# Optimization experiments

Measured on AMD Instinct MI355X. Metric: run time of the kernel, lower is better.

## Reference

```python
import jax, jax.numpy as jnp
import numpy as np
import math

B, C, D, H, W = 1, 64, 16, 16, 16
HEADS = 4
HD = C // HEADS  # head_dim = 16


def conv3d(x, w, b, pad):
    # x: [B,C,D,H,W], w: [O,I,kd,kh,kw], pad: (pd,ph,pw)
    y = jax.lax.conv_general_dilated(
        x, w, window_strides=(1, 1, 1),
        padding=[(p, p) for p in pad],
        dimension_numbers=('NCDHW', 'OIDHW', 'NCDHW'))
    return y + b[None, :, None, None, None]


def setup_inputs() -> dict:
    key = jax.random.key(0)
    ks = jax.random.split(key, 10)
    s = 0.02
    return {
        'x': jax.random.normal(ks[0], (B, C, D, H, W), jnp.float32),
        'gamma': jax.random.normal(ks[1], (1,), jnp.float32),
        'w_sp': jax.random.normal(ks[2], (C, C, 1, 3, 3), jnp.float32) * s,
        'b_sp': jax.random.normal(ks[3], (C,), jnp.float32) * s,
        'w_spec': jax.random.normal(ks[4], (C, C, 3, 1, 1), jnp.float32) * s,
        'b_spec': jax.random.normal(ks[5], (C,), jnp.float32) * s,
        'w_qkv': jax.random.normal(ks[6], (3 * C, C, 1, 1, 1), jnp.float32) * s,
        'b_qkv': jax.random.normal(ks[7], (3 * C,), jnp.float32) * s,
        'w_proj': jax.random.normal(ks[8], (C, C, 1, 1, 1), jnp.float32) * s,
        'b_proj': jax.random.normal(ks[9], (C,), jnp.float32) * s,
    }


def _decay_exponent(dtype):
    # Faithful to the torch permute quirk (requires H == W):
    # exponent[i,j,k,m,n,o] = |i-m| + |j-k| + |n-o|
    dd = jnp.abs(jnp.arange(D)[:, None] - jnp.arange(D)[None, :]).astype(dtype)  # [D,D]
    hh = jnp.abs(jnp.arange(H)[:, None] - jnp.arange(H)[None, :]).astype(dtype)  # [H,H]
    ww = jnp.abs(jnp.arange(W)[:, None] - jnp.arange(W)[None, :]).astype(dtype)  # [W,W]
    return (dd[:, None, None, :, None, None]      # i (axis0), m (axis3)
            + hh[None, :, :, None, None, None]    # j (axis1), k (axis2)
            + ww[None, None, None, None, :, :])   # n (axis4), o (axis5)


def _forward(x, gamma, w_sp, b_sp, w_spec, b_spec, w_qkv, b_qkv, w_proj, b_proj):
    x = conv3d(x, w_sp, b_sp, (0, 1, 1))
    x = conv3d(x, w_spec, b_spec, (1, 0, 0))
    qkv = conv3d(x, w_qkv, b_qkv, (0, 0, 0))
    q, k, v = jnp.split(qkv, 3, axis=1)
    rs = lambda t: t.reshape(B, HEADS, HD, D, H, W)
    q, k, v = rs(q), rs(k), rs(v)

    g = jax.nn.sigmoid(gamma[0])
    decay = g ** _decay_exponent(x.dtype)  # [D,H,W,D,W,W] (H==W)

    # attn[b,h,i,j,k,m,n,o]: (i,j,k)=query D,H,W ; (m,n,o)=key D,H,W
    attn = jnp.einsum('bhdijk,bhdmno->bhijkmno', q, k) / math.sqrt(HD)
    attn = jax.nn.softmax(attn * decay, axis=-1)  # softmax over key-W axis o only
    out = jnp.einsum('bhijkmno,bhdmno->bhdijk', attn, v)
    out = out.reshape(B, C, D, H, W)
    return conv3d(out, w_proj, b_proj, (0, 0, 0))


def reference(x, gamma, w_sp, b_sp, w_spec, b_spec, w_qkv, b_qkv, w_proj, b_proj):
    return _forward(x, gamma, w_sp, b_sp, w_spec, b_spec, w_qkv, b_qkv, w_proj, b_proj)
```

## Files before the change

kernel.cpp:

```cpp
#include <hip/hip_runtime.h>
#include <math.h>

#define CN   262144
#define BTP 196
#define PTP 68

typedef __attribute__((ext_vector_type(8))) short short8;
typedef __attribute__((ext_vector_type(4))) short short4v;
typedef __attribute__((ext_vector_type(4))) float float4v;

static __device__ __forceinline__ unsigned short f2bf(float f) {
    union { float f; unsigned u; } v; v.f = f;
    unsigned r = (v.u + 0x7FFFu + ((v.u >> 16) & 1u)) >> 16;
    return (unsigned short)r;
}

static __device__ __forceinline__ unsigned ld_u32g(const void* p) {
    return __hip_atomic_load((const unsigned*)p, __ATOMIC_RELAXED,
                             __HIP_MEMORY_SCOPE_AGENT);
}
static __device__ __forceinline__ void st_u32g(void* p, unsigned v) {
    __hip_atomic_store((unsigned*)p, v, __ATOMIC_RELAXED,
                       __HIP_MEMORY_SCOPE_AGENT);
}
static __device__ __forceinline__ float ld_f32g(const void* p) {
    return __hip_atomic_load((const float*)p, __ATOMIC_RELAXED,
                             __HIP_MEMORY_SCOPE_AGENT);
}
static __device__ __forceinline__ void st_f32g(void* p, float v) {
    __hip_atomic_store((float*)p, v, __ATOMIC_RELAXED,
                       __HIP_MEMORY_SCOPE_AGENT);
}

#define BAR_LIMIT (1 << 20)

static __device__ __forceinline__ void grid_bar(int* arrive, int* release, int phase) {
    __syncthreads();
    if (blockIdx.x == 0) {
        if (threadIdx.x < 64) {
            if (threadIdx.x == 0)
                __hip_atomic_store(&arrive[0], phase,
                                   __ATOMIC_RELAXED, __HIP_MEMORY_SCOPE_AGENT);
            int base = (int)threadIdx.x * 8 * 32;
            int z = 0; bool done = false;
            while (!done && z < BAR_LIMIT) {
                int mn = phase;
                #pragma unroll
                for (int q = 0; q < 8; ++q) {
                    int a = __hip_atomic_load(&arrive[base + q * 32],
                                              __ATOMIC_RELAXED, __HIP_MEMORY_SCOPE_AGENT);
                    mn = (a < mn) ? a : mn;
                }
                done = (mn >= phase);
                if (!done) __builtin_amdgcn_s_sleep(1);
                ++z;
            }
            __hip_atomic_store(&release[(int)threadIdx.x * 32], phase,
                               __ATOMIC_RELAXED, __HIP_MEMORY_SCOPE_AGENT);
        }
        __syncthreads();
    } else {
        if (threadIdx.x == 0) {
            __hip_atomic_store(&arrive[(int)blockIdx.x * 32], phase,
                               __ATOMIC_RELAXED, __HIP_MEMORY_SCOPE_AGENT);
            int* rel = &release[(blockIdx.x & 63) * 32];
            int z = 0;
            while (__hip_atomic_load(rel, __ATOMIC_RELAXED,
                                     __HIP_MEMORY_SCOPE_AGENT) < phase
                   && z < BAR_LIMIT) {
                __builtin_amdgcn_s_sleep(8);
                ++z;
            }
        }
        __syncthreads();
    }
}

__global__ __launch_bounds__(512, 4) void mega_kernel(
        const float* __restrict__ x, const float* __restrict__ gamma,
        const float* __restrict__ w_sp, const float* __restrict__ b_sp,
        const float* __restrict__ w_spec, const float* __restrict__ b_spec,
        const float* __restrict__ w_qkv, const float* __restrict__ b_qkv,
        const float* __restrict__ w_proj, const float* __restrict__ b_proj,
        float* __restrict__ out, float* ws, int* arrive, int* release) {
    __shared__ __align__(16) unsigned char lds_raw[32896];

    float* y1  = ws;
    unsigned short* wfb = (unsigned short*)(ws + CN);
    float* bfv = ws + CN + 20480;
    unsigned short* qb  = (unsigned short*)(ws + 2 * CN);
    unsigned short* kb  = (unsigned short*)(ws + 2 * CN + CN / 2);
    unsigned short* vtb = (unsigned short*)(ws + 3 * CN);
    float* aoall = ws + 3 * CN + CN / 2;

    if (blockIdx.x < 256) {
        unsigned short* Bt = (unsigned short*)lds_raw;
        int d = blockIdx.x >> 4;
        int h = blockIdx.x & 15;
        int tid = threadIdx.x;
        bool act = tid < 256;
        int px = tid & 15, cig = (tid >> 4) & 15;

        float rcur[12], rnxt[12];
        #define LOAD_CHUNK(dh_, rr)                                            \
            {                                                                  \
                int hh = h + (dh_) - 1;                                        \
                _Pragma("unroll")                                              \
                for (int cc = 0; cc < 4; ++cc) {                               \
                    int ci = cig * 4 + cc;                                     \
                    const float* xr = x + ci * 4096 + d * 256 + hh * 16;       \
                    _Pragma("unroll")                                          \
                    for (int dw = 0; dw < 3; ++dw) {                           \
                        int ww = px + dw - 1;                                  \
                        float v = 0.f;                                         \
                        if (hh >= 0 && hh <= 15 && ww >= 0 && ww <= 15)        \
                            v = xr[ww];                                        \
                        (rr)[cc * 3 + dw] = v;                                 \
                    }                                                          \
                }                                                              \
            }

        if (act) LOAD_CHUNK(0, rcur);

        int wv = (tid >> 6) & 3, lane = tid & 63;
        int quad = lane >> 4, l15 = lane & 15;
        float4v acc = {0.f, 0.f, 0.f, 0.f};
        const float* wrow = w_sp + (wv * 16 + l15) * 576;

        #pragma unroll
        for (int c = 0; c < 3; ++c) {
            __syncthreads();
            if (act) {
                #pragma unroll
                for (int cc = 0; cc < 4; ++cc) {
                    int ci = cig * 4 + cc;
                    Bt[px * BTP + ci * 3 + 0] = f2bf(rcur[cc * 3 + 0]);
                    Bt[px * BTP + ci * 3 + 1] = f2bf(rcur[cc * 3 + 1]);
                    Bt[px * BTP + ci * 3 + 2] = f2bf(rcur[cc * 3 + 2]);
                }
            }
            __syncthreads();
            if (act) {
                if (c < 2) LOAD_CHUNK(c + 1, rnxt);

                const unsigned short* brow = Bt + l15 * BTP + quad * 8;
                #pragma unroll
                for (int ks = 0; ks < 6; ++ks) {
                    short8 af;
                    #pragma unroll
                    for (int j = 0; j < 8; ++j) {
                        int kp = quad * 8 + ks * 32 + j;
                        af[j] = (short)f2bf(wrow[c * 3 + (kp / 3) * 9 + (kp % 3)]);
                    }
                    short4v lo = *(const short4v*)(brow + ks * 32);
                    short4v hi = *(const short4v*)(brow + ks * 32 + 4);
                    short8 bf8 = {lo[0], lo[1], lo[2], lo[3], hi[0], hi[1], hi[2], hi[3]};
                    acc = __builtin_amdgcn_mfma_f32_16x16x32_bf16(af, bf8, acc, 0, 0, 0);
                }
                #pragma unroll
                for (int q2 = 0; q2 < 12; ++q2) rcur[q2] = rnxt[q2];
            }
        }

        if (act) {
            int p = d * 256 + h * 16 + l15;
            #pragma unroll
            for (int r = 0; r < 4; ++r) {
                int co = wv * 16 + quad * 4 + r;
                st_f32g(y1 + co * 4096 + p, acc[r] + b_sp[co]);
            }
        }
        #undef LOAD_CHUNK
    } else {
        int idx = (blockIdx.x - 256) * 512 + threadIdx.x;
        if (idx < 18432) {
            int oc = idx / 96;
            int rp = idx % 96;
            int r0 = rp * 2;
            float s0 = 0.f, s1 = 0.f;
            #pragma unroll 8
            for (int ci = 0; ci < 64; ++ci) {
                float wq = w_qkv[oc * 64 + ci];
                s0 += wq * w_spec[ci * 192 + r0];
                s1 += wq * w_spec[ci * 192 + r0 + 1];
            }
            if (oc < 64) { s0 *= 0.25f; s1 *= 0.25f; }
            st_u32g(wfb + oc * 192 + r0,
                    (unsigned)f2bf(s0) | ((unsigned)f2bf(s1) << 16));
        } else if (idx < 18432 + 192) {
            int j = idx - 18432;
            float t = b_qkv[j];
            for (int ci = 0; ci < 64; ++ci) t += w_qkv[j * 64 + ci] * b_spec[ci];
            if (j < 64) t *= 0.25f;
            st_f32g(bfv + j, t);
        }
    }
    grid_bar(arrive, release, 1);

    if (blockIdx.x < 384) {
        unsigned short* Bt = (unsigned short*)lds_raw;
        int bI  = blockIdx.x;
        int ocg = bI % 3;
        int pq  = (bI / 3) & 7;
        int d   = bI / 24;
        int tid = threadIdx.x;

        {
            int px  = tid & 31;
            int cig = tid >> 5;
            const float* yb = y1 + d * 256 + pq * 32 + px;
            #pragma unroll
            for (int cc = 0; cc < 4; ++cc) {
                int ci = cig * 4 + cc;
                const float* yc = yb + ci * 4096;
                #pragma unroll
                for (int t = 0; t < 3; ++t) {
                    float v = 0.f;
                    if (!((d == 0 && t == 0) || (d == 15 && t == 2)))
                        v = ld_f32g(yc + (t - 1) * 256);
                    Bt[px * BTP + ci * 3 + t] = f2bf(v);
                }
            }
        }

        int wv = tid >> 6, lane = tid & 63;
        int quad = lane >> 4, l15 = lane & 15;
        int Mt = wv >> 1;
        int nt = wv & 1;

        short8 af[6];
        {
            const unsigned* ab = (const unsigned*)(wfb + (ocg * 64 + Mt * 16 + l15) * 192)
                                 + quad * 4;
            #pragma unroll
            for (int ks = 0; ks < 6; ++ks) {
                union { unsigned u[4]; short8 s8; } t;
                #pragma unroll
                for (int q = 0; q < 4; ++q) t.u[q] = ld_u32g(ab + ks * 16 + q);
                af[ks] = t.s8;
            }
        }
        float bias[4];
        #pragma unroll
        for (int r = 0; r < 4; ++r)
            bias[r] = ld_f32g(bfv + ocg * 64 + Mt * 16 + quad * 4 + r);

        __syncthreads();

        float4v czero = {0.f, 0.f, 0.f, 0.f};
        float4v acc = czero;
        {
            const unsigned short* brow = Bt + (nt * 16 + l15) * BTP + quad * 8;
            #pragma unroll
            for (int ks = 0; ks < 6; ++ks) {
                short4v lo = *(const short4v*)(brow + ks * 32);
                short4v hi = *(const short4v*)(brow + ks * 32 + 4);
                short8 bf8 = {lo[0], lo[1], lo[2], lo[3], hi[0], hi[1], hi[2], hi[3]};
                acc = __builtin_amdgcn_mfma_f32_16x16x32_bf16(af[ks], bf8, acc, 0, 0, 0);
            }
        }

        {
            int p = d * 256 + pq * 32 + nt * 16 + l15;
            if (ocg == 2) {
                int h = (p >> 4) & 15, w0 = p & 15;
                int kap = 8 * (w0 >> 2) + 4 * (h & 1) + (w0 & 3);
                unsigned short* dstb = vtb + ((Mt * 16 + d) * 8 + (h >> 1)) * 512
                                           + (quad * 4) * 32;
                int odd = l15 & 1;
                int kap_e = kap - odd;
                #pragma unroll
                for (int r = 0; r < 4; ++r) {
                    unsigned self = f2bf(acc[r] + bias[r]);
                    unsigned other = (unsigned)__shfl_xor((int)self, 1) & 0xFFFFu;
                    unsigned pk = odd ? (other | (self << 16)) : (self | (other << 16));
                    if ((r < 2) == (odd != 0)) continue;
                    st_u32g(dstb + r * 32 + kap_e, pk);
                }
            } else {
                unsigned short* dst = (ocg == 0 ? qb : kb) + Mt * 65536 + p * 16 + quad * 4;
                unsigned t0 = (unsigned)f2bf(acc[0] + bias[0])
                            | ((unsigned)f2bf(acc[1] + bias[1]) << 16);
                unsigned t1 = (unsigned)f2bf(acc[2] + bias[2])
                            | ((unsigned)f2bf(acc[3] + bias[3]) << 16);
                st_u32g(dst, t0);
                st_u32g(dst + 2, t1);
            }
        }
    }
    grid_bar(arrive, release, 2);

    {
        unsigned short* KSH = (unsigned short*)lds_raw;
        unsigned short* VSH = (unsigned short*)lds_raw + 8192;
        float* gp = (float*)(lds_raw + 32768);
        int tid = threadIdx.x;
        if (tid < 32) {
            float g = 1.f / (1.f + __expf(-gamma[0]));
            gp[tid] = __powf(g, (float)tid);
        }
        int wv = tid >> 6, lane = tid & 63;
        int quad = lane >> 4, l15 = lane & 15;
        short8 zero8 = {0, 0, 0, 0, 0, 0, 0, 0};
        float4v czero = {0.f, 0.f, 0.f, 0.f};

        #pragma unroll 1
        for (int it = 0; it < 2; ++it) {
            int bI = blockIdx.x + it * 512;
            int head = bI >> 8;
            int mg   = (bI >> 5) & 7;
            int oct  = bI & 31;
            int t = oct * 8 + wv;
            int i = t >> 4, j = t & 15;

            short8 qf = zero8;
            if (quad < 2) {
                const unsigned* qrow = (const unsigned*)(qb + head * 65536
                                        + (t * 16 + l15) * 16) + quad * 4;
                union { unsigned u[4]; short8 s8; } qt;
                #pragma unroll
                for (int q = 0; q < 4; ++q) qt.u[q] = ld_u32g(qrow + q);
                qf = qt.s8;
            }

            const unsigned* kbu = (const unsigned*)(kb  + head * 65536 + mg * 2 * 4096);
            const unsigned* vbu = (const unsigned*)(vtb + head * 65536 + mg * 2 * 4096);
            unsigned kv[16];
            #pragma unroll
            for (int q = 0; q < 4; ++q) kv[q]      = ld_u32g(kbu + tid * 4 + q);
            #pragma unroll
            for (int q = 0; q < 4; ++q) kv[4 + q]  = ld_u32g(vbu + tid * 4 + q);
            #pragma unroll
            for (int q = 0; q < 4; ++q) kv[8 + q]  = ld_u32g(kbu + 2048 + tid * 4 + q);
            #pragma unroll
            for (int q = 0; q < 4; ++q) kv[12 + q] = ld_u32g(vbu + 2048 + tid * 4 + q);
            __syncthreads();
            #pragma unroll
            for (int q = 0; q < 4; ++q) {
                ((unsigned*)KSH)[tid * 4 + q]        = kv[q];
                ((unsigned*)VSH)[tid * 4 + q]        = kv[4 + q];
                ((unsigned*)(KSH + 4096))[tid * 4 + q] = kv[8 + q];
                ((unsigned*)(VSH + 4096))[tid * 4 + q] = kv[12 + q];
            }
            __syncthreads();

            float wd[4];
            #pragma unroll
            for (int r = 0; r < 4; ++r)
                wd[r] = gp[abs(l15 - (quad * 4 + r))] * 1.4426950408889634f;

            float4v O = czero;
            #pragma unroll
            for (int mm = 0; mm < 2; ++mm) {
                int m = mg * 2 + mm;
                const unsigned short* kk = KSH + mm * 4096;
                const unsigned short* vv = VSH + mm * 4096;
                int eim = abs(i - m);
                #pragma unroll
                for (int np = 0; np < 8; ++np) {
                    union { unsigned u[4]; short8 s8; } a2u;
                    #pragma unroll
                    for (int s = 0; s < 2; ++s) {
                        int n = np * 2 + s;
                        short8 a1 = zero8;
                        if (quad < 2)
                            a1 = *(const short8*)(kk + n * 256 + l15 * 16 + quad * 8);
                        float4v d1 = __builtin_amdgcn_mfma_f32_16x16x32_bf16(a1, qf, czero, 0, 0, 0);
                        float smn = gp[eim + abs(j - n)];
                        float e0 = __builtin_amdgcn_exp2f(d1[0] * smn * wd[0]);
                        float e1 = __builtin_amdgcn_exp2f(d1[1] * smn * wd[1]);
                        float e2 = __builtin_amdgcn_exp2f(d1[2] * smn * wd[2]);
                        float e3 = __builtin_amdgcn_exp2f(d1[3] * smn * wd[3]);
                        float sm = e0 + e1 + e2 + e3;
                        sm += __shfl_xor(sm, 16);
                        sm += __shfl_xor(sm, 32);
                        float inv = __builtin_amdgcn_rcpf(sm);
                        union { float f; unsigned u; } p0, p1, p2, p3;
                        p0.f = e0 * inv; p1.f = e1 * inv;
                        p2.f = e2 * inv; p3.f = e3 * inv;
                        a2u.u[s * 2]     = ((p0.u + 0x8000u) >> 16) | ((p1.u + 0x8000u) & 0xFFFF0000u);
                        a2u.u[s * 2 + 1] = ((p2.u + 0x8000u) >> 16) | ((p3.u + 0x8000u) & 0xFFFF0000u);
                    }
                    short8 b2 = *(const short8*)(vv + np * 512 + l15 * 32 + quad * 8);
                    O = __builtin_amdgcn_mfma_f32_16x16x32_bf16(a2u.s8, b2, O, 0, 0, 0);
                }
            }

            float* aop = aoall + mg * CN + (head * 16 + l15) * 4096 + t * 16 + quad * 4;
            #pragma unroll
            for (int r = 0; r < 4; ++r) st_f32g(aop + r, O[r]);
        }
    }
    grid_bar(arrive, release, 3);

    if (blockIdx.x < 256) {
        unsigned short* Bt = (unsigned short*)lds_raw;
        int d   = blockIdx.x >> 4;
        int p16 = blockIdx.x & 15;
        int tid = threadIdx.x;
        bool act = tid < 256;

        if (act) {
            int px = tid & 15, cig = (tid >> 4) & 15;
            int gbase = d * 256 + p16 * 16 + px;
            #pragma unroll
            for (int cc = 0; cc < 4; ++cc) {
                int ci = cig * 4 + cc;
                int ga = ci * 4096 + gbase;
                float v = 0.f;
                #pragma unroll
                for (int k = 0; k < 8; ++k) v += ld_f32g(aoall + k * CN + ga);
                Bt[px * PTP + ci] = f2bf(v);
            }
        }
        __syncthreads();

        if (act) {
            int wv = (tid >> 6) & 3, lane = tid & 63;
            int quad = lane >> 4, l15 = lane & 15;
            float4v czero = {0.f, 0.f, 0.f, 0.f};
            float4v acc = czero;

            short8 af[2];
            const float* wsrc = w_proj + (wv * 16 + l15) * 64 + quad * 8;
            #pragma unroll
            for (int ks = 0; ks < 2; ++ks) {
                float4 wa = *(const float4*)(wsrc + ks * 32);
                float4 wb = *(const float4*)(wsrc + ks * 32 + 4);
                short8 a8 = {(short)f2bf(wa.x), (short)f2bf(wa.y), (short)f2bf(wa.z),
                             (short)f2bf(wa.w), (short)f2bf(wb.x), (short)f2bf(wb.y),
                             (short)f2bf(wb.z), (short)f2bf(wb.w)};
                af[ks] = a8;
            }
            const unsigned short* brow = Bt + l15 * PTP + quad * 8;
            #pragma unroll
            for (int ks = 0; ks < 2; ++ks) {
                short4v lo = *(const short4v*)(brow + ks * 32);
                short4v hi = *(const short4v*)(brow + ks * 32 + 4);
                short8 bf8 = {lo[0], lo[1], lo[2], lo[3], hi[0], hi[1], hi[2], hi[3]};
                acc = __builtin_amdgcn_mfma_f32_16x16x32_bf16(af[ks], bf8, acc, 0, 0, 0);
            }

            int p = d * 256 + p16 * 16 + l15;
            #pragma unroll
            for (int r = 0; r < 4; ++r) {
                int oc = wv * 16 + quad * 4 + r;
                out[oc * 4096 + p] = acc[r] + b_proj[oc];
            }
        }
    }
}

extern "C" void kernel_launch(void* const* d_in, const int* in_sizes, int n_in,
                              void* d_out, int out_size, void* d_ws, size_t ws_size,
                              hipStream_t stream) {
    const float* x      = (const float*)d_in[0];
    const float* gamma  = (const float*)d_in[1];
    const float* w_sp   = (const float*)d_in[2];
    const float* b_sp   = (const float*)d_in[3];
    const float* w_spec = (const float*)d_in[4];
    const float* b_spec = (const float*)d_in[5];
    const float* w_qkv  = (const float*)d_in[6];
    const float* b_qkv  = (const float*)d_in[7];
    const float* w_proj = (const float*)d_in[8];
    const float* b_proj = (const float*)d_in[9];
    float* out = (float*)d_out;
    float* ws = (float*)d_ws;

    int* arrive  = (int*)(ws + 12 * CN);
    int* release = arrive + 512 * 32;
    hipMemsetAsync(arrive, 0, (512 + 64) * 128, stream);

    mega_kernel<<<dim3(512), dim3(512), 0, stream>>>(
        x, gamma, w_sp, b_sp, w_spec, b_spec, w_qkv, b_qkv, w_proj, b_proj,
        out, ws, arrive, release);
}
```

Measured before the change: 146.1 us.

## Restructure attention stage to one pass per block with four key slices and plain loads

```diff
diff --git a/kernel.cpp b/kernel.cpp
--- a/kernel.cpp
+++ b/kernel.cpp
@@ -15,17 +15,13 @@
     return (unsigned short)r;
 }
 
-static __device__ __forceinline__ unsigned ld_u32g(const void* p) {
-    return __hip_atomic_load((const unsigned*)p, __ATOMIC_RELAXED,
-                             __HIP_MEMORY_SCOPE_AGENT);
-}
 static __device__ __forceinline__ void st_u32g(void* p, unsigned v) {
     __hip_atomic_store((unsigned*)p, v, __ATOMIC_RELAXED,
                        __HIP_MEMORY_SCOPE_AGENT);
 }
-static __device__ __forceinline__ float ld_f32g(const void* p) {
-    return __hip_atomic_load((const float*)p, __ATOMIC_RELAXED,
-                             __HIP_MEMORY_SCOPE_AGENT);
+static __device__ __forceinline__ void st_u64g(void* p, unsigned long long v) {
+    __hip_atomic_store((unsigned long long*)p, v, __ATOMIC_RELAXED,
+                       __HIP_MEMORY_SCOPE_AGENT);
 }
 static __device__ __forceinline__ void st_f32g(void* p, float v) {
     __hip_atomic_store((float*)p, v, __ATOMIC_RELAXED,
@@ -68,7 +64,7 @@
             while (__hip_atomic_load(rel, __ATOMIC_RELAXED,
                                      __HIP_MEMORY_SCOPE_AGENT) < phase
                    && z < BAR_LIMIT) {
-                __builtin_amdgcn_s_sleep(8);
+                __builtin_amdgcn_s_sleep(2);
                 ++z;
             }
         }
@@ -217,7 +213,7 @@
                 for (int t = 0; t < 3; ++t) {
                     float v = 0.f;
                     if (!((d == 0 && t == 0) || (d == 15 && t == 2)))
-                        v = ld_f32g(yc + (t - 1) * 256);
+                        v = yc[(t - 1) * 256];
                     Bt[px * BTP + ci * 3 + t] = f2bf(v);
                 }
             }
@@ -230,20 +226,13 @@
 
         short8 af[6];
         {
-            const unsigned* ab = (const unsigned*)(wfb + (ocg * 64 + Mt * 16 + l15) * 192)
-                                 + quad * 4;
-            #pragma unroll
-            for (int ks = 0; ks < 6; ++ks) {
-                union { unsigned u[4]; short8 s8; } t;
-                #pragma unroll
-                for (int q = 0; q < 4; ++q) t.u[q] = ld_u32g(ab + ks * 16 + q);
-                af[ks] = t.s8;
-            }
+            const unsigned short* ab = wfb + (ocg * 64 + Mt * 16 + l15) * 192 + quad * 8;
+            #pragma unroll
+            for (int ks = 0; ks < 6; ++ks) af[ks] = *(const short8*)(ab + ks * 32);
         }
         float bias[4];
         #pragma unroll
-        for (int r = 0; r < 4; ++r)
-            bias[r] = ld_f32g(bfv + ocg * 64 + Mt * 16 + quad * 4 + r);
+        for (int r = 0; r < 4; ++r) bias[r] = bfv[ocg * 64 + Mt * 16 + quad * 4 + r];
 
         __syncthreads();
 
@@ -283,8 +272,7 @@
                             | ((unsigned)f2bf(acc[1] + bias[1]) << 16);
                 unsigned t1 = (unsigned)f2bf(acc[2] + bias[2])
                             | ((unsigned)f2bf(acc[3] + bias[3]) << 16);
-                st_u32g(dst, t0);
-                st_u32g(dst + 2, t1);
+                st_u64g(dst, (unsigned long long)t0 | ((unsigned long long)t1 << 32));
             }
         }
     }
@@ -292,104 +280,85 @@
 
     {
         unsigned short* KSH = (unsigned short*)lds_raw;
-        unsigned short* VSH = (unsigned short*)lds_raw + 8192;
         float* gp = (float*)(lds_raw + 32768);
         int tid = threadIdx.x;
+        int bI = blockIdx.x;
+        int head = bI >> 7;
+        int mg   = (bI >> 5) & 3;
+        int oct  = bI & 31;
+
         if (tid < 32) {
             float g = 1.f / (1.f + __expf(-gamma[0]));
             gp[tid] = __powf(g, (float)tid);
         }
+
         int wv = tid >> 6, lane = tid & 63;
         int quad = lane >> 4, l15 = lane & 15;
+        int t = oct * 8 + wv;
+        int i = t >> 4, j = t & 15;
+
         short8 zero8 = {0, 0, 0, 0, 0, 0, 0, 0};
         float4v czero = {0.f, 0.f, 0.f, 0.f};
-
+        short8 qf = zero8;
+        if (quad < 2)
+            qf = *(const short8*)(qb + head * 65536 + (t * 16 + l15) * 16 + quad * 8);
+
+        {
+            const float4* kbh = (const float4*)(kb + head * 65536 + mg * 4 * 4096);
+            #pragma unroll
+            for (int q = 0; q < 4; ++q)
+                ((float4*)KSH)[q * 512 + tid] = kbh[q * 512 + tid];
+        }
+        __syncthreads();
+
+        float wd[4];
+        #pragma unroll
+        for (int r = 0; r < 4; ++r)
+            wd[r] = gp[abs(l15 - (quad * 4 + r))] * 1.4426950408889634f;
+
+        float4v O = czero;
         #pragma unroll 1
-        for (int it = 0; it < 2; ++it) {
-            int bI = blockIdx.x + it * 512;
-            int head = bI >> 8;
-            int mg   = (bI >> 5) & 7;
-            int oct  = bI & 31;
-            int t = oct * 8 + wv;
-            int i = t >> 4, j = t & 15;
-
-            short8 qf = zero8;
-            if (quad < 2) {
-                const unsigned* qrow = (const unsigned*)(qb + head * 65536
-                                        + (t * 16 + l15) * 16) + quad * 4;
-                union { unsigned u[4]; short8 s8; } qt;
-                #pragma unroll
-                for (int q = 0; q < 4; ++q) qt.u[q] = ld_u32g(qrow + q);
-                qf = qt.s8;
-            }
-
-            const unsigned* kbu = (const unsigned*)(kb  + head * 65536 + mg * 2 * 4096);
-            const unsigned* vbu = (const unsigned*)(vtb + head * 65536 + mg * 2 * 4096);
-            unsigned kv[16];
-            #pragma unroll
-            for (int q = 0; q < 4; ++q) kv[q]      = ld_u32g(kbu + tid * 4 + q);
-            #pragma unroll
-            for (int q = 0; q < 4; ++q) kv[4 + q]  = ld_u32g(vbu + tid * 4 + q);
-            #pragma unroll
-            for (int q = 0; q < 4; ++q) kv[8 + q]  = ld_u32g(kbu + 2048 + tid * 4 + q);
-            #pragma unroll
-            for (int q = 0; q < 4; ++q) kv[12 + q] = ld_u32g(vbu + 2048 + tid * 4 + q);
-            __syncthreads();
-            #pragma unroll
-            for (int q = 0; q < 4; ++q) {
-                ((unsigned*)KSH)[tid * 4 + q]        = kv[q];
-                ((unsigned*)VSH)[tid * 4 + q]        = kv[4 + q];
-                ((unsigned*)(KSH + 4096))[tid * 4 + q] = kv[8 + q];
-                ((unsigned*)(VSH + 4096))[tid * 4 + q] = kv[12 + q];
-            }
-            __syncthreads();
-
-            float wd[4];
-            #pragma unroll
-            for (int r = 0; r < 4; ++r)
-                wd[r] = gp[abs(l15 - (quad * 4 + r))] * 1.4426950408889634f;
-
-            float4v O = czero;
-            #pragma unroll
-            for (int mm = 0; mm < 2; ++mm) {
-                int m = mg * 2 + mm;
-                const unsigned short* kk = KSH + mm * 4096;
-                const unsigned short* vv = VSH + mm * 4096;
-                int eim = abs(i - m);
-                #pragma unroll
-                for (int np = 0; np < 8; ++np) {
-                    union { unsigned u[4]; short8 s8; } a2u;
-                    #pragma unroll
-                    for (int s = 0; s < 2; ++s) {
-                        int n = np * 2 + s;
-                        short8 a1 = zero8;
-                        if (quad < 2)
-                            a1 = *(const short8*)(kk + n * 256 + l15 * 16 + quad * 8);
-                        float4v d1 = __builtin_amdgcn_mfma_f32_16x16x32_bf16(a1, qf, czero, 0, 0, 0);
-                        float smn = gp[eim + abs(j - n)];
-                        float e0 = __builtin_amdgcn_exp2f(d1[0] * smn * wd[0]);
-                        float e1 = __builtin_amdgcn_exp2f(d1[1] * smn * wd[1]);
-                        float e2 = __builtin_amdgcn_exp2f(d1[2] * smn * wd[2]);
-                        float e3 = __builtin_amdgcn_exp2f(d1[3] * smn * wd[3]);
-                        float sm = e0 + e1 + e2 + e3;
-                        sm += __shfl_xor(sm, 16);
-                        sm += __shfl_xor(sm, 32);
-                        float inv = __builtin_amdgcn_rcpf(sm);
-                        union { float f; unsigned u; } p0, p1, p2, p3;
-                        p0.f = e0 * inv; p1.f = e1 * inv;
-                        p2.f = e2 * inv; p3.f = e3 * inv;
-                        a2u.u[s * 2]     = ((p0.u + 0x8000u) >> 16) | ((p1.u + 0x8000u) & 0xFFFF0000u);
-                        a2u.u[s * 2 + 1] = ((p2.u + 0x8000u) >> 16) | ((p3.u + 0x8000u) & 0xFFFF0000u);
-                    }
-                    short8 b2 = *(const short8*)(vv + np * 512 + l15 * 32 + quad * 8);
-                    O = __builtin_amdgcn_mfma_f32_16x16x32_bf16(a2u.s8, b2, O, 0, 0, 0);
-                }
-            }
-
-            float* aop = aoall + mg * CN + (head * 16 + l15) * 4096 + t * 16 + quad * 4;
-            #pragma unroll
-            for (int r = 0; r < 4; ++r) st_f32g(aop + r, O[r]);
-        }
+        for (int mm = 0; mm < 4; ++mm) {
+            int m = mg * 4 + mm;
+            const unsigned short* kk = KSH + mm * 4096;
+            const unsigned short* vvg = vtb + head * 65536 + m * 4096;
+            int eim = abs(i - m);
+            #pragma unroll
+            for (int np = 0; np < 8; ++np) {
+                union { unsigned u[4]; short8 s8; } a2u;
+                #pragma unroll
+                for (int s = 0; s < 2; ++s) {
+                    int n = np * 2 + s;
+                    short8 a1 = zero8;
+                    if (quad < 2)
+                        a1 = *(const short8*)(kk + n * 256 + l15 * 16 + quad * 8);
+                    float4v d1 = __builtin_amdgcn_mfma_f32_16x16x32_bf16(a1, qf, czero, 0, 0, 0);
+                    float smn = gp[eim + abs(j - n)];
+                    float e0 = __builtin_amdgcn_exp2f(d1[0] * smn * wd[0]);
+                    float e1 = __builtin_amdgcn_exp2f(d1[1] * smn * wd[1]);
+                    float e2 = __builtin_amdgcn_exp2f(d1[2] * smn * wd[2]);
+                    float e3 = __builtin_amdgcn_exp2f(d1[3] * smn * wd[3]);
+                    float sm = e0 + e1 + e2 + e3;
+                    sm += __shfl_xor(sm, 16);
+                    sm += __shfl_xor(sm, 32);
+                    float inv = __builtin_amdgcn_rcpf(sm);
+                    union { float f; unsigned u; } p0, p1, p2, p3;
+                    p0.f = e0 * inv; p1.f = e1 * inv;
+                    p2.f = e2 * inv; p3.f = e3 * inv;
+                    a2u.u[s * 2]     = ((p0.u + 0x8000u) >> 16) | ((p1.u + 0x8000u) & 0xFFFF0000u);
+                    a2u.u[s * 2 + 1] = ((p2.u + 0x8000u) >> 16) | ((p3.u + 0x8000u) & 0xFFFF0000u);
+                }
+                short8 b2 = *(const short8*)(vvg + np * 512 + l15 * 32 + quad * 8);
+                O = __builtin_amdgcn_mfma_f32_16x16x32_bf16(a2u.s8, b2, O, 0, 0, 0);
+            }
+        }
+
+        float* aop = aoall + mg * CN + (head * 16 + l15) * 4096 + t * 16 + quad * 4;
+        union { float f[2]; unsigned long long u; } o01, o23;
+        o01.f[0] = O[0]; o01.f[1] = O[1];
+        o23.f[0] = O[2]; o23.f[1] = O[3];
+        st_u64g(aop, o01.u);
+        st_u64g(aop + 2, o23.u);
     }
     grid_bar(arrive, release, 3);
 
@@ -409,7 +378,7 @@
                 int ga = ci * 4096 + gbase;
                 float v = 0.f;
                 #pragma unroll
-                for (int k = 0; k < 8; ++k) v += ld_f32g(aoall + k * CN + ga);
+                for (int k = 0; k < 4; ++k) v += aoall[k * CN + ga];
                 Bt[px * PTP + ci] = f2bf(v);
             }
         }
```

Measured after the change: 131.0 us. 1.12x faster.
